# Kernel optimization log

Measured on AMD Instinct MI355X. Metric: run time of the kernel, lower is better.

## Reference

```python
import jax, jax.numpy as jnp
import numpy as np

WEIGHT_SCALE = 0.01      # weight_scale buffer
WEIGHT_ZP = 8            # weight_zero_point buffer
BIAS_SCALE = 0.01 * 0.047  # bias_scale = weight_scale * activation_scale (from_float)
OUT_FEATURES = 4096
IN_FEATURES = 4096


def setup_inputs() -> dict:
    key = jax.random.key(0)
    k1, k2, k3 = jax.random.split(key, 3)
    x = jax.random.normal(k1, (8, 2048, IN_FEATURES), dtype=jnp.float32)
    # packed uint8 bytes, two 4-bit weights per byte; stored as int32 (values 0..255)
    packed_weight = jax.random.randint(k2, (OUT_FEATURES, IN_FEATURES // 2), 0, 256, dtype=jnp.int32)
    quantized_bias = jax.random.randint(k3, (OUT_FEATURES,), -500, 500, dtype=jnp.int32)
    return {"x": x, "packed_weight": packed_weight, "quantized_bias": quantized_bias}


def _dequantize_weights(packed_weight):
    # low nibble -> even input column, high nibble -> odd input column
    low = packed_weight & 15          # [O, I/2]
    high = (packed_weight >> 4) & 15  # [O, I/2]
    q = jnp.stack([low, high], axis=-1).reshape(OUT_FEATURES, IN_FEATURES)
    return WEIGHT_SCALE * (q.astype(jnp.float32) - WEIGHT_ZP)


def reference(x, packed_weight, quantized_bias):
    W = _dequantize_weights(packed_weight)                 # [O, I]
    b = BIAS_SCALE * quantized_bias.astype(jnp.float32)    # [O]
    # F.linear: x @ W.T + b
    return jnp.einsum('bsi,oi->bso', x, W) + b
```

## Files before the change

kernel.cpp:

```cpp
#include <hip/hip_runtime.h>


typedef __bf16 bf16x8 __attribute__((ext_vector_type(8)));
typedef float f32x4 __attribute__((ext_vector_type(4)));
typedef unsigned short u16;
typedef u16 u16x4 __attribute__((ext_vector_type(4)));
typedef u16 u16x8 __attribute__((ext_vector_type(8)));

static constexpr int Kdim = 4096;
static constexpr int Ndim = 4096;
static constexpr int BM = 256, BN = 256, BK = 64;
static constexpr int NKT = Kdim / BK;
static constexpr int TBUF = BM * BK;

__device__ __forceinline__ u16 f2bf(float f) {
  union { float f; unsigned u; } c; c.f = f;
  unsigned u = c.u;
  return (u16)((u + 0x7FFFu + ((u >> 16) & 1u)) >> 16);
}

__global__ __launch_bounds__(256) void cvt_x_kernel(const float* __restrict__ x,
                                                    u16* __restrict__ xb, int n4) {
  int stride = gridDim.x * blockDim.x;
  for (int i = blockIdx.x * blockDim.x + threadIdx.x; i < n4; i += stride) {
    float4 v = reinterpret_cast<const float4*>(x)[i];
    u16x4 o;
    o.x = f2bf(v.x); o.y = f2bf(v.y); o.z = f2bf(v.z); o.w = f2bf(v.w);
    reinterpret_cast<u16x4*>(xb)[i] = o;
  }
}

__global__ __launch_bounds__(256) void dequant_w_kernel(const int* __restrict__ pw,
                                                        u16* __restrict__ wb, int n4) {
  int stride = gridDim.x * blockDim.x;
  for (int i = blockIdx.x * blockDim.x + threadIdx.x; i < n4; i += stride) {
    int4 v = reinterpret_cast<const int4*>(pw)[i];
    int a[4] = {v.x, v.y, v.z, v.w};
    u16x8 o;
#pragma unroll
    for (int j = 0; j < 4; ++j) {
      o[2 * j]     = f2bf((float)((a[j] & 15) - 8));
      o[2 * j + 1] = f2bf((float)(((a[j] >> 4) & 15) - 8));
    }
    reinterpret_cast<u16x8*>(wb)[i] = o;
  }
}

__device__ __forceinline__ void gload16(const u16* g, const u16* l) {
  __builtin_amdgcn_global_load_lds(
      (const __attribute__((address_space(1))) void*)g,
      (__attribute__((address_space(3))) void*)l,
      16, 0, 0);
}

__global__ __launch_bounds__(512, 2) void gemm_kernel(const u16* __restrict__ A,
                                                      const u16* __restrict__ B,
                                                      const int* __restrict__ qbias,
                                                      float* __restrict__ C,
                                                      int Ntiles) {
  extern __shared__ u16 smem[];
  u16* As = smem;
  u16* Bs = smem + 3 * TBUF;

  const int tid = threadIdx.x;
  const int lane = tid & 63;
  const int wave = tid >> 6;
  const int wm = wave >> 2, wn = wave & 3;

  const int cpx = gridDim.x >> 3;
  const int bid = blockIdx.x;
  const int swz = (bid & 7) * cpx + (bid >> 3);
  const int bx = swz % Ntiles;
  const int by = swz / Ntiles;
  const int m0 = by * BM, n0 = bx * BN;

  const int srow = tid >> 3;
  const int fcol = (((tid & 7) ^ (srow & 7)) << 3);
  const u16* pa[4];
  const u16* pb[4];
#pragma unroll
  for (int i = 0; i < 4; ++i) {
    pa[i] = A + (size_t)(m0 + i * 64 + srow) * Kdim + fcol;
    pb[i] = B + (size_t)(n0 + i * 64 + srow) * Kdim + fcol;
  }
  const int wbase = (tid & 0x1C0) * 8;

  const int e0 = ((lane >> 4) ^ (lane & 7)) << 3;
  const int e1 = e0 ^ 32;
  const int arow = (wm * 128 + (lane & 15)) * 64;
  const int brow = (wn * 64 + (lane & 15)) * 64;

  f32x4 acc[8][4] = {};

#pragma unroll
  for (int i = 0; i < 4; ++i) gload16(pb[i], Bs + i * 4096 + wbase);
#pragma unroll
  for (int i = 0; i < 4; ++i) gload16(pa[i], As + i * 4096 + wbase);
#pragma unroll
  for (int i = 0; i < 4; ++i) gload16(pa[i] + BK, As + TBUF + i * 4096 + wbase);
  asm volatile("s_waitcnt vmcnt(4)" ::: "memory");
  __builtin_amdgcn_s_barrier();

  int rbuf = 0;
  for (int t = 0; t < NKT; ++t) {
    const u16* aL = As + rbuf * TBUF;
    const u16* bL = Bs + (t & 1) * TBUF;
    const u16* aW = As + ((rbuf + 2) % 3) * TBUF;
    const u16* bW = Bs + ((t + 1) & 1) * TBUF;
    const bool stb = (t + 1) < NKT;
    const bool sta = (t + 2) < NKT;
    const int kob = (t + 1) * BK;
    const int koa = (t + 2) * BK;

    bf16x8 af[4], bf[4][2];

#define PHASE_TAIL(ACC_BASE, KH)                                              \
    __builtin_amdgcn_s_barrier();                                             \
    asm volatile("s_waitcnt lgkmcnt(0)" ::: "memory");                        \
    __builtin_amdgcn_sched_barrier(0);                                        \
    __builtin_amdgcn_s_setprio(1);                                            \
    _Pragma("unroll")                                                         \
    for (int m = 0; m < 4; ++m)                                               \
      _Pragma("unroll")                                                       \
      for (int n = 0; n < 4; ++n)                                             \
        acc[(ACC_BASE) + m][n] = __builtin_amdgcn_mfma_f32_16x16x32_bf16(     \
            af[m], bf[n][KH], acc[(ACC_BASE) + m][n], 0, 0, 0);               \
    __builtin_amdgcn_s_setprio(0);                                            \
    __builtin_amdgcn_sched_barrier(0);                                        \
    __builtin_amdgcn_s_barrier();

#pragma unroll
    for (int m = 0; m < 4; ++m)
      af[m] = *(const bf16x8*)(aL + arow + m * 1024 + e0);
#pragma unroll
    for (int n = 0; n < 4; ++n) {
      bf[n][0] = *(const bf16x8*)(bL + brow + n * 1024 + e0);
      bf[n][1] = *(const bf16x8*)(bL + brow + n * 1024 + e1);
    }
    if (stb) { gload16(pb[0] + kob, bW + 0 * 4096 + wbase);
               gload16(pb[1] + kob, bW + 1 * 4096 + wbase); }
    PHASE_TAIL(0, 0)

#pragma unroll
    for (int m = 0; m < 4; ++m)
      af[m] = *(const bf16x8*)(aL + arow + m * 1024 + e1);
    if (stb) { gload16(pb[2] + kob, bW + 2 * 4096 + wbase);
               gload16(pb[3] + kob, bW + 3 * 4096 + wbase); }
    PHASE_TAIL(0, 1)

#pragma unroll
    for (int m = 0; m < 4; ++m)
      af[m] = *(const bf16x8*)(aL + arow + 4096 + m * 1024 + e0);
    if (sta) { gload16(pa[0] + koa, aW + 0 * 4096 + wbase);
               gload16(pa[1] + koa, aW + 1 * 4096 + wbase); }
    PHASE_TAIL(4, 0)

#pragma unroll
    for (int m = 0; m < 4; ++m)
      af[m] = *(const bf16x8*)(aL + arow + 4096 + m * 1024 + e1);
    if (sta) { gload16(pa[2] + koa, aW + 2 * 4096 + wbase);
               gload16(pa[3] + koa, aW + 3 * 4096 + wbase); }
    __builtin_amdgcn_s_barrier();
    asm volatile("s_waitcnt lgkmcnt(0)" ::: "memory");
    __builtin_amdgcn_sched_barrier(0);
    __builtin_amdgcn_s_setprio(1);
#pragma unroll
    for (int m = 0; m < 4; ++m)
#pragma unroll
      for (int n = 0; n < 4; ++n)
        acc[4 + m][n] = __builtin_amdgcn_mfma_f32_16x16x32_bf16(
            af[m], bf[n][1], acc[4 + m][n], 0, 0, 0);
    __builtin_amdgcn_s_setprio(0);
    __builtin_amdgcn_sched_barrier(0);

    if (sta)      asm volatile("s_waitcnt vmcnt(4)" ::: "memory");
    else if (stb) asm volatile("s_waitcnt vmcnt(0)" ::: "memory");
    __builtin_amdgcn_s_barrier();

    rbuf = (rbuf == 2) ? 0 : rbuf + 1;
#undef PHASE_TAIL
  }

  const float wscale = 0.01f;
  const float bscale = (float)(0.01 * 0.047);
  const int col0 = n0 + wn * 64 + (lane & 15);
  const int row0 = m0 + wm * 128 + ((lane >> 4) << 2);
#pragma unroll
  for (int n = 0; n < 4; ++n) {
    const int col = col0 + n * 16;
    const float bias = bscale * (float)qbias[col];
#pragma unroll
    for (int m = 0; m < 8; ++m) {
      const int rr = row0 + m * 16;
#pragma unroll
      for (int j = 0; j < 4; ++j)
        C[(size_t)(rr + j) * Ndim + col] = wscale * acc[m][n][j] + bias;
    }
  }
}

extern "C" void kernel_launch(void* const* d_in, const int* in_sizes, int n_in,
                              void* d_out, int out_size, void* d_ws, size_t ws_size,
                              hipStream_t stream) {
  const float* x  = (const float*)d_in[0];
  const int*   pw = (const int*)d_in[1];
  const int*   qb = (const int*)d_in[2];
  float* out = (float*)d_out;

  const int M = in_sizes[0] / Kdim;

  u16* xb = (u16*)d_ws;
  u16* wb = (u16*)((char*)d_ws + (size_t)M * Kdim * 2);

  cvt_x_kernel<<<2048, 256, 0, stream>>>(x, xb, M * Kdim / 4);
  dequant_w_kernel<<<1024, 256, 0, stream>>>(pw, wb, Ndim * Kdim / 8);

  const int Ntiles = Ndim / BN;
  const int nwg = (M / BM) * Ntiles;
  static const size_t lds_bytes = 5u * TBUF * sizeof(u16);
  (void)hipFuncSetAttribute((const void*)gemm_kernel,
                            hipFuncAttributeMaxDynamicSharedMemorySize,
                            (int)lds_bytes);
  gemm_kernel<<<nwg, 512, lds_bytes, stream>>>(xb, wb, qb, out, Ntiles);
}
```

Measured before the change: 550.4 us.

## Drop intra-iteration barriers and double-buffer A fragments with partial LDS waits

```diff
diff --git a/kernel.cpp b/kernel.cpp
--- a/kernel.cpp
+++ b/kernel.cpp
@@ -112,55 +112,65 @@
     const int kob = (t + 1) * BK;
     const int koa = (t + 2) * BK;
 
-    bf16x8 af[4], bf[4][2];
-
-#define PHASE_TAIL(ACC_BASE, KH)                                              \
-    __builtin_amdgcn_s_barrier();                                             \
-    asm volatile("s_waitcnt lgkmcnt(0)" ::: "memory");                        \
-    __builtin_amdgcn_sched_barrier(0);                                        \
-    __builtin_amdgcn_s_setprio(1);                                            \
-    _Pragma("unroll")                                                         \
-    for (int m = 0; m < 4; ++m)                                               \
-      _Pragma("unroll")                                                       \
-      for (int n = 0; n < 4; ++n)                                             \
-        acc[(ACC_BASE) + m][n] = __builtin_amdgcn_mfma_f32_16x16x32_bf16(     \
-            af[m], bf[n][KH], acc[(ACC_BASE) + m][n], 0, 0, 0);               \
-    __builtin_amdgcn_s_setprio(0);                                            \
-    __builtin_amdgcn_sched_barrier(0);                                        \
-    __builtin_amdgcn_s_barrier();
-
-#pragma unroll
-    for (int m = 0; m < 4; ++m)
-      af[m] = *(const bf16x8*)(aL + arow + m * 1024 + e0);
-#pragma unroll
-    for (int n = 0; n < 4; ++n) {
+    bf16x8 a0[4], a1[4], bf[4][2];
+
+#pragma unroll
+    for (int m = 0; m < 4; ++m)
+      a0[m] = *(const bf16x8*)(aL + arow + m * 1024 + e0);
+#pragma unroll
+    for (int n = 0; n < 4; ++n)
       bf[n][0] = *(const bf16x8*)(bL + brow + n * 1024 + e0);
+#pragma unroll
+    for (int n = 0; n < 4; ++n)
       bf[n][1] = *(const bf16x8*)(bL + brow + n * 1024 + e1);
-    }
+
+#pragma unroll
+    for (int m = 0; m < 4; ++m)
+      a1[m] = *(const bf16x8*)(aL + arow + 4096 + m * 1024 + e0);
     if (stb) { gload16(pb[0] + kob, bW + 0 * 4096 + wbase);
                gload16(pb[1] + kob, bW + 1 * 4096 + wbase); }
-    PHASE_TAIL(0, 0)
-
-#pragma unroll
-    for (int m = 0; m < 4; ++m)
-      af[m] = *(const bf16x8*)(aL + arow + m * 1024 + e1);
+    asm volatile("s_waitcnt lgkmcnt(4)" ::: "memory");
+    __builtin_amdgcn_sched_barrier(0);
+    __builtin_amdgcn_s_setprio(1);
+#pragma unroll
+    for (int m = 0; m < 4; ++m)
+#pragma unroll
+      for (int n = 0; n < 4; ++n)
+        acc[m][n] = __builtin_amdgcn_mfma_f32_16x16x32_bf16(a0[m], bf[n][0], acc[m][n], 0, 0, 0);
+    __builtin_amdgcn_s_setprio(0);
+
+#pragma unroll
+    for (int m = 0; m < 4; ++m)
+      a0[m] = *(const bf16x8*)(aL + arow + m * 1024 + e1);
     if (stb) { gload16(pb[2] + kob, bW + 2 * 4096 + wbase);
                gload16(pb[3] + kob, bW + 3 * 4096 + wbase); }
-    PHASE_TAIL(0, 1)
-
-#pragma unroll
-    for (int m = 0; m < 4; ++m)
-      af[m] = *(const bf16x8*)(aL + arow + 4096 + m * 1024 + e0);
+    asm volatile("s_waitcnt lgkmcnt(4)" ::: "memory");
+    __builtin_amdgcn_sched_barrier(0);
+    __builtin_amdgcn_s_setprio(1);
+#pragma unroll
+    for (int m = 0; m < 4; ++m)
+#pragma unroll
+      for (int n = 0; n < 4; ++n)
+        acc[4 + m][n] = __builtin_amdgcn_mfma_f32_16x16x32_bf16(a1[m], bf[n][0], acc[4 + m][n], 0, 0, 0);
+    __builtin_amdgcn_s_setprio(0);
+
+#pragma unroll
+    for (int m = 0; m < 4; ++m)
+      a1[m] = *(const bf16x8*)(aL + arow + 4096 + m * 1024 + e1);
     if (sta) { gload16(pa[0] + koa, aW + 0 * 4096 + wbase);
                gload16(pa[1] + koa, aW + 1 * 4096 + wbase); }
-    PHASE_TAIL(4, 0)
-
-#pragma unroll
-    for (int m = 0; m < 4; ++m)
-      af[m] = *(const bf16x8*)(aL + arow + 4096 + m * 1024 + e1);
+    asm volatile("s_waitcnt lgkmcnt(4)" ::: "memory");
+    __builtin_amdgcn_sched_barrier(0);
+    __builtin_amdgcn_s_setprio(1);
+#pragma unroll
+    for (int m = 0; m < 4; ++m)
+#pragma unroll
+      for (int n = 0; n < 4; ++n)
+        acc[m][n] = __builtin_amdgcn_mfma_f32_16x16x32_bf16(a0[m], bf[n][1], acc[m][n], 0, 0, 0);
+    __builtin_amdgcn_s_setprio(0);
+
     if (sta) { gload16(pa[2] + koa, aW + 2 * 4096 + wbase);
                gload16(pa[3] + koa, aW + 3 * 4096 + wbase); }
-    __builtin_amdgcn_s_barrier();
     asm volatile("s_waitcnt lgkmcnt(0)" ::: "memory");
     __builtin_amdgcn_sched_barrier(0);
     __builtin_amdgcn_s_setprio(1);
@@ -168,8 +178,7 @@
     for (int m = 0; m < 4; ++m)
 #pragma unroll
       for (int n = 0; n < 4; ++n)
-        acc[4 + m][n] = __builtin_amdgcn_mfma_f32_16x16x32_bf16(
-            af[m], bf[n][1], acc[4 + m][n], 0, 0, 0);
+        acc[4 + m][n] = __builtin_amdgcn_mfma_f32_16x16x32_bf16(a1[m], bf[n][1], acc[4 + m][n], 0, 0, 0);
     __builtin_amdgcn_s_setprio(0);
     __builtin_amdgcn_sched_barrier(0);
 
@@ -178,7 +187,6 @@
     __builtin_amdgcn_s_barrier();
 
     rbuf = (rbuf == 2) ? 0 : rbuf + 1;
-#undef PHASE_TAIL
   }
 
   const float wscale = 0.01f;
```

Result: faster. 539.6 us (-2.0%).

## Switch GEMM to 32x32x16 MFMA with double-buffered LDS fragment reads

Applied to the files above, without the earlier changes.

```diff
diff --git a/kernel.cpp b/kernel.cpp
--- a/kernel.cpp
+++ b/kernel.cpp
@@ -2,7 +2,7 @@
 
 
 typedef __bf16 bf16x8 __attribute__((ext_vector_type(8)));
-typedef float f32x4 __attribute__((ext_vector_type(4)));
+typedef float f32x16 __attribute__((ext_vector_type(16)));
 typedef unsigned short u16;
 typedef u16 u16x4 __attribute__((ext_vector_type(4)));
 typedef u16 u16x8 __attribute__((ext_vector_type(8)));
@@ -85,12 +85,16 @@
   }
   const int wbase = (tid & 0x1C0) * 8;
 
-  const int e0 = ((lane >> 4) ^ (lane & 7)) << 3;
-  const int e1 = e0 ^ 32;
-  const int arow = (wm * 128 + (lane & 15)) * 64;
-  const int brow = (wn * 64 + (lane & 15)) * 64;
-
-  f32x4 acc[8][4] = {};
+  const int kb = lane >> 5;
+  const int lx = lane & 7;
+  const int es0 = ((0 + kb) ^ lx) << 3;
+  const int es1 = ((2 + kb) ^ lx) << 3;
+  const int es2 = ((4 + kb) ^ lx) << 3;
+  const int es3 = ((6 + kb) ^ lx) << 3;
+  const int ar0 = (wm * 128 + (lane & 31)) * 64;
+  const int br0 = (wn * 64 + (lane & 31)) * 64;
+
+  f32x16 acc[4][2] = {};
 
 #pragma unroll
   for (int i = 0; i < 4; ++i) gload16(pb[i], Bs + i * 4096 + wbase);
@@ -100,6 +104,25 @@
   for (int i = 0; i < 4; ++i) gload16(pa[i] + BK, As + TBUF + i * 4096 + wbase);
   asm volatile("s_waitcnt vmcnt(4)" ::: "memory");
   __builtin_amdgcn_s_barrier();
+
+#define READS(AF, BF, ES)                                                     \
+    _Pragma("unroll")                                                         \
+    for (int mt = 0; mt < 4; ++mt)                                            \
+      AF[mt] = *(const bf16x8*)(aL + ar0 + mt * 2048 + (ES));                 \
+    _Pragma("unroll")                                                         \
+    for (int nt = 0; nt < 2; ++nt)                                            \
+      BF[nt] = *(const bf16x8*)(bL + br0 + nt * 2048 + (ES));
+
+#define MFMAS(AF, BF)                                                         \
+    __builtin_amdgcn_sched_barrier(0);                                        \
+    __builtin_amdgcn_s_setprio(1);                                            \
+    _Pragma("unroll")                                                         \
+    for (int mt = 0; mt < 4; ++mt)                                            \
+      _Pragma("unroll")                                                       \
+      for (int nt = 0; nt < 2; ++nt)                                          \
+        acc[mt][nt] = __builtin_amdgcn_mfma_f32_32x32x16_bf16(                \
+            AF[mt], BF[nt], acc[mt][nt], 0, 0, 0);                            \
+    __builtin_amdgcn_s_setprio(0);
 
   int rbuf = 0;
   for (int t = 0; t < NKT; ++t) {
@@ -112,65 +135,32 @@
     const int kob = (t + 1) * BK;
     const int koa = (t + 2) * BK;
 
-    bf16x8 af[4], bf[4][2];
-
-#define PHASE_TAIL(ACC_BASE, KH)                                              \
-    __builtin_amdgcn_s_barrier();                                             \
-    asm volatile("s_waitcnt lgkmcnt(0)" ::: "memory");                        \
-    __builtin_amdgcn_sched_barrier(0);                                        \
-    __builtin_amdgcn_s_setprio(1);                                            \
-    _Pragma("unroll")                                                         \
-    for (int m = 0; m < 4; ++m)                                               \
-      _Pragma("unroll")                                                       \
-      for (int n = 0; n < 4; ++n)                                             \
-        acc[(ACC_BASE) + m][n] = __builtin_amdgcn_mfma_f32_16x16x32_bf16(     \
-            af[m], bf[n][KH], acc[(ACC_BASE) + m][n], 0, 0, 0);               \
-    __builtin_amdgcn_s_setprio(0);                                            \
-    __builtin_amdgcn_sched_barrier(0);                                        \
-    __builtin_amdgcn_s_barrier();
-
-#pragma unroll
-    for (int m = 0; m < 4; ++m)
-      af[m] = *(const bf16x8*)(aL + arow + m * 1024 + e0);
-#pragma unroll
-    for (int n = 0; n < 4; ++n) {
-      bf[n][0] = *(const bf16x8*)(bL + brow + n * 1024 + e0);
-      bf[n][1] = *(const bf16x8*)(bL + brow + n * 1024 + e1);
-    }
+    bf16x8 afA[4], bfA[2], afB[4], bfB[2];
+
+    READS(afA, bfA, es0)
+
+    READS(afB, bfB, es1)
     if (stb) { gload16(pb[0] + kob, bW + 0 * 4096 + wbase);
                gload16(pb[1] + kob, bW + 1 * 4096 + wbase); }
-    PHASE_TAIL(0, 0)
-
-#pragma unroll
-    for (int m = 0; m < 4; ++m)
-      af[m] = *(const bf16x8*)(aL + arow + m * 1024 + e1);
+    asm volatile("s_waitcnt lgkmcnt(6)" ::: "memory");
+    MFMAS(afA, bfA)
+
+    READS(afA, bfA, es2)
     if (stb) { gload16(pb[2] + kob, bW + 2 * 4096 + wbase);
                gload16(pb[3] + kob, bW + 3 * 4096 + wbase); }
-    PHASE_TAIL(0, 1)
-
-#pragma unroll
-    for (int m = 0; m < 4; ++m)
-      af[m] = *(const bf16x8*)(aL + arow + 4096 + m * 1024 + e0);
+    asm volatile("s_waitcnt lgkmcnt(6)" ::: "memory");
+    MFMAS(afB, bfB)
+
+    READS(afB, bfB, es3)
     if (sta) { gload16(pa[0] + koa, aW + 0 * 4096 + wbase);
                gload16(pa[1] + koa, aW + 1 * 4096 + wbase); }
-    PHASE_TAIL(4, 0)
-
-#pragma unroll
-    for (int m = 0; m < 4; ++m)
-      af[m] = *(const bf16x8*)(aL + arow + 4096 + m * 1024 + e1);
+    asm volatile("s_waitcnt lgkmcnt(6)" ::: "memory");
+    MFMAS(afA, bfA)
+
     if (sta) { gload16(pa[2] + koa, aW + 2 * 4096 + wbase);
                gload16(pa[3] + koa, aW + 3 * 4096 + wbase); }
-    __builtin_amdgcn_s_barrier();
     asm volatile("s_waitcnt lgkmcnt(0)" ::: "memory");
-    __builtin_amdgcn_sched_barrier(0);
-    __builtin_amdgcn_s_setprio(1);
-#pragma unroll
-    for (int m = 0; m < 4; ++m)
-#pragma unroll
-      for (int n = 0; n < 4; ++n)
-        acc[4 + m][n] = __builtin_amdgcn_mfma_f32_16x16x32_bf16(
-            af[m], bf[n][1], acc[4 + m][n], 0, 0, 0);
-    __builtin_amdgcn_s_setprio(0);
+    MFMAS(afB, bfB)
     __builtin_amdgcn_sched_barrier(0);
 
     if (sta)      asm volatile("s_waitcnt vmcnt(4)" ::: "memory");
@@ -178,23 +168,25 @@
     __builtin_amdgcn_s_barrier();
 
     rbuf = (rbuf == 2) ? 0 : rbuf + 1;
-#undef PHASE_TAIL
-  }
+  }
+#undef READS
+#undef MFMAS
 
   const float wscale = 0.01f;
   const float bscale = (float)(0.01 * 0.047);
-  const int col0 = n0 + wn * 64 + (lane & 15);
-  const int row0 = m0 + wm * 128 + ((lane >> 4) << 2);
-#pragma unroll
-  for (int n = 0; n < 4; ++n) {
-    const int col = col0 + n * 16;
+  const int colb = n0 + wn * 64 + (lane & 31);
+  const int rowb = m0 + wm * 128 + ((lane >> 5) << 2);
+#pragma unroll
+  for (int nt = 0; nt < 2; ++nt) {
+    const int col = colb + nt * 32;
     const float bias = bscale * (float)qbias[col];
 #pragma unroll
-    for (int m = 0; m < 8; ++m) {
-      const int rr = row0 + m * 16;
-#pragma unroll
-      for (int j = 0; j < 4; ++j)
-        C[(size_t)(rr + j) * Ndim + col] = wscale * acc[m][n][j] + bias;
+    for (int mt = 0; mt < 4; ++mt) {
+#pragma unroll
+      for (int reg = 0; reg < 16; ++reg) {
+        const int row = rowb + mt * 32 + (reg & 3) + 8 * (reg >> 2);
+        C[(size_t)row * Ndim + col] = wscale * acc[mt][nt][reg] + bias;
+      }
     }
   }
 }
```

After: 548.0 us. Within noise of the previous version (-0.4%).

## Restructure GEMM pipeline to double-buffered A/B with two-tile unrolled schedule

Applied to the files above, without the earlier changes.

```diff
diff --git a/kernel.cpp b/kernel.cpp
--- a/kernel.cpp
+++ b/kernel.cpp
@@ -60,7 +60,7 @@
                                                       int Ntiles) {
   extern __shared__ u16 smem[];
   u16* As = smem;
-  u16* Bs = smem + 3 * TBUF;
+  u16* Bs = smem + 2 * TBUF;
 
   const int tid = threadIdx.x;
   const int lane = tid & 63;
@@ -91,30 +91,28 @@
   const int brow = (wn * 64 + (lane & 15)) * 64;
 
   f32x4 acc[8][4] = {};
+  bf16x8 af[4], bq[2][4];
 
 #pragma unroll
   for (int i = 0; i < 4; ++i) gload16(pb[i], Bs + i * 4096 + wbase);
 #pragma unroll
   for (int i = 0; i < 4; ++i) gload16(pa[i], As + i * 4096 + wbase);
-#pragma unroll
-  for (int i = 0; i < 4; ++i) gload16(pa[i] + BK, As + TBUF + i * 4096 + wbase);
+  gload16(pa[0] + BK, As + TBUF + 0 * 4096 + wbase);
+  gload16(pa[2] + BK, As + TBUF + 2 * 4096 + wbase);
+  gload16(pb[0] + BK, Bs + TBUF + 0 * 4096 + wbase);
+  gload16(pb[1] + BK, Bs + TBUF + 1 * 4096 + wbase);
   asm volatile("s_waitcnt vmcnt(4)" ::: "memory");
   __builtin_amdgcn_s_barrier();
 
-  int rbuf = 0;
-  for (int t = 0; t < NKT; ++t) {
-    const u16* aL = As + rbuf * TBUF;
-    const u16* bL = Bs + (t & 1) * TBUF;
-    const u16* aW = As + ((rbuf + 2) % 3) * TBUF;
-    const u16* bW = Bs + ((t + 1) & 1) * TBUF;
-    const bool stb = (t + 1) < NKT;
-    const bool sta = (t + 2) < NKT;
-    const int kob = (t + 1) * BK;
-    const int koa = (t + 2) * BK;
-
-    bf16x8 af[4], bf[4][2];
-
-#define PHASE_TAIL(ACC_BASE, KH)                                              \
+#define RD_A(BUF, MH, E)                                                      \
+    _Pragma("unroll")                                                         \
+    for (int m = 0; m < 4; ++m)                                               \
+      af[m] = *(const bf16x8*)((BUF) + arow + (MH) * 4096 + m * 1024 + (E));
+#define RD_B(KH, BUF, E)                                                      \
+    _Pragma("unroll")                                                         \
+    for (int n = 0; n < 4; ++n)                                               \
+      bq[KH][n] = *(const bf16x8*)((BUF) + brow + n * 1024 + (E));
+#define MF(BASE, KH)                                                          \
     __builtin_amdgcn_s_barrier();                                             \
     asm volatile("s_waitcnt lgkmcnt(0)" ::: "memory");                        \
     __builtin_amdgcn_sched_barrier(0);                                        \
@@ -123,63 +121,78 @@
     for (int m = 0; m < 4; ++m)                                               \
       _Pragma("unroll")                                                       \
       for (int n = 0; n < 4; ++n)                                             \
-        acc[(ACC_BASE) + m][n] = __builtin_amdgcn_mfma_f32_16x16x32_bf16(     \
-            af[m], bf[n][KH], acc[(ACC_BASE) + m][n], 0, 0, 0);               \
-    __builtin_amdgcn_s_setprio(0);                                            \
-    __builtin_amdgcn_sched_barrier(0);                                        \
-    __builtin_amdgcn_s_barrier();
-
-#pragma unroll
-    for (int m = 0; m < 4; ++m)
-      af[m] = *(const bf16x8*)(aL + arow + m * 1024 + e0);
-#pragma unroll
-    for (int n = 0; n < 4; ++n) {
-      bf[n][0] = *(const bf16x8*)(bL + brow + n * 1024 + e0);
-      bf[n][1] = *(const bf16x8*)(bL + brow + n * 1024 + e1);
-    }
-    if (stb) { gload16(pb[0] + kob, bW + 0 * 4096 + wbase);
-               gload16(pb[1] + kob, bW + 1 * 4096 + wbase); }
-    PHASE_TAIL(0, 0)
-
-#pragma unroll
-    for (int m = 0; m < 4; ++m)
-      af[m] = *(const bf16x8*)(aL + arow + m * 1024 + e1);
-    if (stb) { gload16(pb[2] + kob, bW + 2 * 4096 + wbase);
-               gload16(pb[3] + kob, bW + 3 * 4096 + wbase); }
-    PHASE_TAIL(0, 1)
-
-#pragma unroll
-    for (int m = 0; m < 4; ++m)
-      af[m] = *(const bf16x8*)(aL + arow + 4096 + m * 1024 + e0);
-    if (sta) { gload16(pa[0] + koa, aW + 0 * 4096 + wbase);
-               gload16(pa[1] + koa, aW + 1 * 4096 + wbase); }
-    PHASE_TAIL(4, 0)
-
-#pragma unroll
-    for (int m = 0; m < 4; ++m)
-      af[m] = *(const bf16x8*)(aL + arow + 4096 + m * 1024 + e1);
-    if (sta) { gload16(pa[2] + koa, aW + 2 * 4096 + wbase);
-               gload16(pa[3] + koa, aW + 3 * 4096 + wbase); }
-    __builtin_amdgcn_s_barrier();
-    asm volatile("s_waitcnt lgkmcnt(0)" ::: "memory");
-    __builtin_amdgcn_sched_barrier(0);
-    __builtin_amdgcn_s_setprio(1);
-#pragma unroll
-    for (int m = 0; m < 4; ++m)
-#pragma unroll
-      for (int n = 0; n < 4; ++n)
-        acc[4 + m][n] = __builtin_amdgcn_mfma_f32_16x16x32_bf16(
-            af[m], bf[n][1], acc[4 + m][n], 0, 0, 0);
+        acc[(BASE) + m][n] = __builtin_amdgcn_mfma_f32_16x16x32_bf16(         \
+            af[m], bq[KH][n], acc[(BASE) + m][n], 0, 0, 0);                   \
     __builtin_amdgcn_s_setprio(0);
-    __builtin_amdgcn_sched_barrier(0);
-
-    if (sta)      asm volatile("s_waitcnt vmcnt(4)" ::: "memory");
-    else if (stb) asm volatile("s_waitcnt vmcnt(0)" ::: "memory");
-    __builtin_amdgcn_s_barrier();
-
-    rbuf = (rbuf == 2) ? 0 : rbuf + 1;
-#undef PHASE_TAIL
-  }
+
+  for (int j = 0; j < NKT / 2; ++j) {
+    const int t = 2 * j;
+    const bool s2 = (t + 2) < NKT;
+    const bool s3 = (t + 3) < NKT;
+    const int k1 = (t + 1) * BK, k2 = (t + 2) * BK, k3 = (t + 3) * BK;
+    const u16* aL0 = As;            const u16* bL0 = Bs;
+    const u16* aL1 = As + TBUF;     const u16* bL1 = Bs + TBUF;
+
+    RD_A(aL0, 0, e0)
+    RD_B(0, bL0, e0)
+    gload16(pb[2] + k1, Bs + TBUF + 2 * 4096 + wbase);
+    gload16(pb[3] + k1, Bs + TBUF + 3 * 4096 + wbase);
+    gload16(pa[1] + k1, As + TBUF + 1 * 4096 + wbase);
+    gload16(pa[3] + k1, As + TBUF + 3 * 4096 + wbase);
+    MF(0, 0)
+    __builtin_amdgcn_s_barrier();
+
+    RD_A(aL0, 0, e1)
+    RD_B(1, bL0, e1)
+    MF(0, 1)
+    __builtin_amdgcn_s_barrier();
+
+    RD_A(aL0, 1, e0)
+    if (s2) { gload16(pb[0] + k2, Bs + 0 * 4096 + wbase);
+              gload16(pb[1] + k2, Bs + 1 * 4096 + wbase); }
+    MF(4, 0)
+    __builtin_amdgcn_s_barrier();
+
+    RD_A(aL0, 1, e1)
+    if (s2) { gload16(pb[2] + k2, Bs + 2 * 4096 + wbase);
+              gload16(pb[3] + k2, Bs + 3 * 4096 + wbase); }
+    MF(4, 1)
+    if (s2) { asm volatile("s_waitcnt vmcnt(6)" ::: "memory"); }
+    else    { asm volatile("s_waitcnt vmcnt(2)" ::: "memory"); }
+    __builtin_amdgcn_s_barrier();
+
+    RD_A(aL1, 0, e0)
+    RD_B(0, bL1, e0)
+    if (s2) { gload16(pa[0] + k2, As + 0 * 4096 + wbase);
+              gload16(pa[1] + k2, As + 1 * 4096 + wbase);
+              gload16(pa[2] + k2, As + 2 * 4096 + wbase);
+              gload16(pa[3] + k2, As + 3 * 4096 + wbase); }
+    MF(0, 0)
+    __builtin_amdgcn_s_barrier();
+
+    RD_A(aL1, 0, e1)
+    RD_B(1, bL1, e1)
+    MF(0, 1)
+    if (s2) { asm volatile("s_waitcnt vmcnt(8)" ::: "memory"); }
+    else    { asm volatile("s_waitcnt vmcnt(0)" ::: "memory"); }
+    __builtin_amdgcn_s_barrier();
+
+    RD_A(aL1, 1, e0)
+    if (s3) { gload16(pa[0] + k3, As + TBUF + 0 * 4096 + wbase);
+              gload16(pa[2] + k3, As + TBUF + 2 * 4096 + wbase); }
+    MF(4, 0)
+    __builtin_amdgcn_s_barrier();
+
+    RD_A(aL1, 1, e1)
+    if (s3) { gload16(pb[0] + k3, Bs + TBUF + 0 * 4096 + wbase);
+              gload16(pb[1] + k3, Bs + TBUF + 1 * 4096 + wbase); }
+    MF(4, 1)
+    if (s3) { asm volatile("s_waitcnt vmcnt(4)" ::: "memory"); }
+    __builtin_amdgcn_s_barrier();
+  }
+#undef RD_A
+#undef RD_B
+#undef MF
 
   const float wscale = 0.01f;
   const float bscale = (float)(0.01 * 0.047);
@@ -217,7 +230,7 @@
 
   const int Ntiles = Ndim / BN;
   const int nwg = (M / BM) * Ntiles;
-  static const size_t lds_bytes = 5u * TBUF * sizeof(u16);
+  static const size_t lds_bytes = 4u * TBUF * sizeof(u16);
   (void)hipFuncSetAttribute((const void*)gemm_kernel,
                             hipFuncAttributeMaxDynamicSharedMemorySize,
                             (int)lds_bytes);
```

Result: no change. 549.9 us (-0.1%).
